# Kernel optimization log

Measured on AMD Instinct MI355X. Metric: run time of the kernel, lower is better.

## Reference

```python
import jax, jax.numpy as jnp
import numpy as np

HIDDEN = 1280
NUM_HEADS = 16
HEAD_DIM = HIDDEN // NUM_HEADS  # 80
ROPE_DIM = HEAD_DIM // 2        # 40
THETA = 10000.0
SEQ = 3072


def setup_inputs() -> dict:
    key = jax.random.key(0)
    ks = jax.random.split(key, 6)
    hidden_states = jax.random.normal(ks[0], (SEQ, HIDDEN), dtype=jnp.float32)
    position_ids = jax.random.randint(ks[1], (SEQ, 2), 0, 64, dtype=jnp.int32)
    qkv_w = jax.random.normal(ks[2], (HIDDEN, 3 * HIDDEN), dtype=jnp.float32) * (HIDDEN ** -0.5)
    qkv_b = jax.random.normal(ks[3], (3 * HIDDEN,), dtype=jnp.float32) * 0.02
    o_w = jax.random.normal(ks[4], (HIDDEN, HIDDEN), dtype=jnp.float32) * (HIDDEN ** -0.5)
    o_b = jax.random.normal(ks[5], (HIDDEN,), dtype=jnp.float32) * 0.02
    return {"hidden_states": hidden_states, "position_ids": position_ids,
            "qkv_w": qkv_w, "qkv_b": qkv_b, "o_w": o_w, "o_b": o_b}


def _rotate_half(x):
    x1, x2 = jnp.split(x, 2, axis=-1)
    return jnp.concatenate([-x2, x1], axis=-1)


def reference(hidden_states, position_ids, qkv_w, qkv_b, o_w, o_b):
    seq_len = hidden_states.shape[0]
    # fused QKV projection
    qkv = hidden_states @ qkv_w + qkv_b                     # (S, 3*H*D)
    qkv = qkv.reshape(seq_len, 3, NUM_HEADS, HEAD_DIM)
    q, k, v = qkv[:, 0], qkv[:, 1], qkv[:, 2]               # each (S, h, d)
    # 2D RoPE: inv_freq over rope dim = head_dim // 2
    inv_freq = 1.0 / (THETA ** (jnp.arange(0, ROPE_DIM, 2, dtype=jnp.float32) / ROPE_DIM))
    pos = position_ids.astype(jnp.float32)
    h_freqs = jnp.outer(pos[:, 0], inv_freq)                # (S, rope/2)
    w_freqs = jnp.outer(pos[:, 1], inv_freq)                # (S, rope/2)
    freqs = jnp.concatenate([h_freqs, w_freqs], axis=-1)    # (S, rope)
    emb = jnp.concatenate([freqs, freqs], axis=-1)          # (S, head_dim)
    cos = jnp.cos(emb)[:, None, :]                          # (S, 1, d)
    sin = jnp.sin(emb)[:, None, :]
    q = q * cos + _rotate_half(q) * sin
    k = k * cos + _rotate_half(k) * sin
    # manual attention
    scaling = HEAD_DIM ** -0.5
    attn = jnp.einsum('qhd,khd->hqk', q * scaling, k)       # (h, S, S)
    attn = jax.nn.softmax(attn, axis=-1)
    out = jnp.einsum('hqk,khd->qhd', attn, v)               # (S, h, d)
    out = out.reshape(seq_len, HIDDEN)
    return out @ o_w + o_b
```

## Files before the change

### kernel.cpp

```cpp
#include <hip/hip_runtime.h>

#define SEQ  3072
#define HID  1280
#define NH   16
#define HD   80
#define NQKV 3840

typedef unsigned short u16;
typedef unsigned int u32;
typedef __attribute__((ext_vector_type(8))) short short8;
typedef __attribute__((ext_vector_type(4))) float floatx4;

__device__ __forceinline__ u16 f2bf(float x) {
    u32 u = __float_as_uint(x);
    u += 0x7fffu + ((u >> 16) & 1u);
    return (u16)(u >> 16);
}
__device__ __forceinline__ float bf2f(u16 b) {
    return __uint_as_float(((u32)b) << 16);
}
__device__ __forceinline__ u32 pack2bf(float a, float b) {
    u32 ua = __float_as_uint(a) + 0x8000u;
    u32 ub = __float_as_uint(b) + 0x8000u;
    return (ua >> 16) | (ub & 0xffff0000u);
}

typedef const __attribute__((address_space(1))) unsigned int* gp1_t;
typedef __attribute__((address_space(3))) unsigned int* lp3_t;
__device__ __forceinline__ void gld16(const void* g, void* l) {
    __builtin_amdgcn_global_load_lds((gp1_t)g, (lp3_t)l, 16, 0, 0);
}

__device__ __forceinline__ int swz_qk(int c, int r) {
    return (c < 8) ? (c ^ (r & 7)) : (8 + ((c - 8) ^ (r & 3)));
}

__global__ void rope_tables_k(const int* __restrict__ pos, float* __restrict__ cosb,
                              float* __restrict__ sinb) {
    int s = blockIdx.x;
    int j = threadIdx.x;
    if (j >= 40) return;
    float p = (float)((j < 20) ? pos[s * 2] : pos[s * 2 + 1]);
    int i = (j < 20) ? j : j - 20;
    float inv = powf(10000.0f, -(float)i / 20.0f);
    float a = p * inv;
    cosb[s * 40 + j] = cosf(a);
    sinb[s * 40 + j] = sinf(a);
}

__global__ void cast_bf16_k(const float* __restrict__ x, u16* __restrict__ hi, int n) {
    int i = blockIdx.x * 256 + threadIdx.x;
    if (i >= n) return;
    hi[i] = f2bf(x[i]);
}

__global__ void transpose_cast_k(const float* __restrict__ w, u16* __restrict__ thi,
                                 int K, int N) {
    __shared__ float tile[32][33];
    int n0 = blockIdx.x * 32, k0 = blockIdx.y * 32;
    int c = threadIdx.x & 31, r8 = threadIdx.x >> 5;
    for (int rr = r8; rr < 32; rr += 8)
        tile[rr][c] = w[(size_t)(k0 + rr) * N + n0 + c];
    __syncthreads();
    for (int rr = r8; rr < 32; rr += 8)
        thi[(size_t)(n0 + rr) * K + k0 + c] = f2bf(tile[c][rr]);
}

__global__ __launch_bounds__(256, 3) void gemm_bf16_k(
    const u16* __restrict__ A, const u16* __restrict__ B,
    const float* __restrict__ bias, float* __restrict__ C,
    int M, int N, int K) {
    __shared__ u16 lA[128 * 64], lB[128 * 64];
    const int t = threadIdx.x, lane = t & 63, w = t >> 6;
    const int qi = lane & 15, quad = lane >> 4;
    const int m0 = blockIdx.y * 128, n0 = blockIdx.x * 128;
    const int wm = (w >> 1) * 64, wn = (w & 1) * 64;

    floatx4 acc[4][4];
    for (int mi = 0; mi < 4; mi++)
        for (int ni = 0; ni < 4; ni++) acc[mi][ni] = (floatx4){0.f, 0.f, 0.f, 0.f};

    const int rg = lane >> 3;
    const int ce = ((lane & 7) ^ rg) * 8;
    size_t gA[4], gB[4];
    for (int g = 0; g < 4; g++) {
        int row = w * 32 + g * 8 + rg;
        gA[g] = (size_t)(m0 + row) * K + ce;
        gB[g] = (size_t)(n0 + row) * K + ce;
    }

    for (int k0 = 0; k0 < K; k0 += 64) {
        for (int g = 0; g < 4; g++) {
            gld16(A + gA[g] + k0, &lA[(w * 32 + g * 8) * 64]);
            gld16(B + gB[g] + k0, &lB[(w * 32 + g * 8) * 64]);
        }
        __syncthreads();
        short8 af[4][2], bf[4][2];
        for (int mi = 0; mi < 4; mi++) {
            int row = wm + mi * 16 + qi;
            for (int kh = 0; kh < 2; kh++)
                af[mi][kh] = *(const short8*)&lA[row * 64 + (((kh * 4 + quad) ^ (row & 7)) << 3)];
        }
        for (int ni = 0; ni < 4; ni++) {
            int row = wn + ni * 16 + qi;
            for (int kh = 0; kh < 2; kh++)
                bf[ni][kh] = *(const short8*)&lB[row * 64 + (((kh * 4 + quad) ^ (row & 7)) << 3)];
        }
        for (int mi = 0; mi < 4; mi++)
            for (int ni = 0; ni < 4; ni++) {
                acc[mi][ni] = __builtin_amdgcn_mfma_f32_16x16x32_bf16(af[mi][0], bf[ni][0], acc[mi][ni], 0, 0, 0);
                acc[mi][ni] = __builtin_amdgcn_mfma_f32_16x16x32_bf16(af[mi][1], bf[ni][1], acc[mi][ni], 0, 0, 0);
            }
        __syncthreads();
    }
    for (int mi = 0; mi < 4; mi++)
        for (int ni = 0; ni < 4; ni++) {
            int col = n0 + wn + ni * 16 + qi;
            int rowb = m0 + wm + mi * 16 + quad * 4;
            float b = bias[col];
            for (int r = 0; r < 4; r++)
                C[(size_t)(rowb + r) * N + col] = acc[mi][ni][r] + b;
        }
}

__global__ void pack_qkv_k(const float* __restrict__ qkv, const float* __restrict__ cosb,
                           const float* __restrict__ sinb,
                           u16* __restrict__ Qs, u16* __restrict__ Ks, u16* __restrict__ Vs) {
    __shared__ float lv[80 * 65];
    const int t = threadIdx.x;
    const int h = blockIdx.y, s0 = blockIdx.x * 64;
    const float scale = 0.11180339887498949f;

    for (int i = t; i < 64 * 40; i += 256) {
        int rl = i / 40, j = i % 40;
        int s = s0 + rl;
        float c = cosb[s * 40 + j], sn = sinb[s * 40 + j];
        const float* qb = qkv + (size_t)s * NQKV + h * HD;
        float q1 = qb[j], q2 = qb[j + 40];
        size_t base = (size_t)(h * SEQ + s) * 96;
        int j2 = j + 40;
        size_t o1 = base + swz_qk(j >> 3, s) * 8 + (j & 7);
        size_t o2 = base + swz_qk(j2 >> 3, s) * 8 + (j2 & 7);
        Qs[o1] = f2bf((q1 * c - q2 * sn) * scale);
        Qs[o2] = f2bf((q2 * c + q1 * sn) * scale);
        const float* kb = qb + HID;
        float k1 = kb[j], k2 = kb[j + 40];
        Ks[o1] = f2bf(k1 * c - k2 * sn);
        Ks[o2] = f2bf(k2 * c + k1 * sn);
    }
    for (int i = t; i < 64 * 16; i += 256) {
        int rl = i / 16, jj = 80 + i % 16;
        int s = s0 + rl;
        size_t o = (size_t)(h * SEQ + s) * 96 + swz_qk(jj >> 3, s) * 8 + (jj & 7);
        Qs[o] = 0;
        Ks[o] = 0;
    }
    for (int i = t; i < 64 * 80; i += 256) {
        int rl = i / 80, d = i % 80;
        lv[d * 65 + rl] = qkv[(size_t)(s0 + rl) * NQKV + 2 * HID + h * HD + d];
    }
    __syncthreads();
    for (int i = t; i < 80 * 64; i += 256) {
        int d = i / 64, c2l = i % 64;
        int pc = ((c2l >> 3) ^ (d & 7));
        Vs[((size_t)h * HD + d) * SEQ + s0 + pc * 8 + (c2l & 7)] = f2bf(lv[d * 65 + c2l]);
    }
}

__global__ __launch_bounds__(256, 3) void attn_k(
    const u16* __restrict__ Qs, const u16* __restrict__ Ks, const u16* __restrict__ Vs,
    float* __restrict__ Op, float* __restrict__ lp) {
    __shared__ u16 kbuf[2][6144];
    __shared__ u16 vbuf[2][5120];
    __shared__ u16 pls[4][1024];

    const int t = threadIdx.x, lane = t & 63, w = t >> 6;
    const int qi = lane & 15, quad = lane >> 4;
    const int h = blockIdx.y, q0 = blockIdx.x * 128, ksp = blockIdx.z;
    const int kc0 = ksp * (SEQ / 2);
    u16* const kflat = &kbuf[0][0];

    {
        const u16* Qt = Qs + (size_t)(h * SEQ + q0) * 96;
        for (int j = 0; j < 6; j++) {
            int o = (w * 6 + j) * 512;
            gld16(Qt + o + lane * 8, kflat + o);
        }
    }
    __syncthreads();
    short8 bq[2][3];
    for (int qg = 0; qg < 2; qg++) {
        int row = w * 32 + qg * 16 + qi;
        for (int k3 = 0; k3 < 3; k3++) {
            int p = (k3 < 2) ? ((4 * k3 + quad) ^ (qi & 7)) : (8 + (quad ^ (qi & 3)));
            bq[qg][k3] = *(const short8*)&kflat[(row * 12 + p) * 8];
        }
    }
    __syncthreads();

    float l_lane[2] = {0.f, 0.f};
    floatx4 acco[2][5];
    for (int qg = 0; qg < 2; qg++)
        for (int dt = 0; dt < 5; dt++) acco[qg][dt] = (floatx4){0.f, 0.f, 0.f, 0.f};

    auto stage = [&](int it, int buf) {
        int kc = kc0 + it * 64;
        const u16* Kt = Ks + (size_t)(h * SEQ + kc) * 96;
        for (int j = 0; j < 3; j++) {
            int o = (w * 3 + j) * 512;
            gld16(Kt + o + lane * 8, &kbuf[buf][o]);
        }
        const u16* Vt = Vs + (size_t)h * HD * SEQ + kc;
        for (int i = w; i < 10; i += 4) {
            int p16 = i * 64 + lane;
            int d = p16 >> 3, pc = p16 & 7;
            gld16(Vt + (size_t)d * SEQ + pc * 8, &vbuf[buf][i * 512]);
        }
    };
    stage(0, 0);
    __syncthreads();

    const int NT = (SEQ / 2) / 64;
    char* const myp = (char*)&pls[w][0];
    for (int it = 0; it < NT; it++) {
        int cur = it & 1;
        if (it + 1 < NT) stage(it + 1, cur ^ 1);
        const u16* kb = &kbuf[cur][0];
        const u16* vb = &vbuf[cur][0];
        for (int c2 = 0; c2 < 2; c2++) {
            for (int ktl = 0; ktl < 2; ktl++) {
                int kt = c2 * 2 + ktl;
                int arow = kt * 16 + qi;
                short8 ak[3];
                for (int k3 = 0; k3 < 3; k3++) {
                    int p = (k3 < 2) ? ((4 * k3 + quad) ^ (qi & 7)) : (8 + (quad ^ (qi & 3)));
                    ak[k3] = *(const short8*)&kb[(arow * 12 + p) * 8];
                }
                for (int qg = 0; qg < 2; qg++) {
                    floatx4 s = (floatx4){0.f, 0.f, 0.f, 0.f};
                    s = __builtin_amdgcn_mfma_f32_16x16x32_bf16(ak[0], bq[qg][0], s, 0, 0, 0);
                    s = __builtin_amdgcn_mfma_f32_16x16x32_bf16(ak[1], bq[qg][1], s, 0, 0, 0);
                    s = __builtin_amdgcn_mfma_f32_16x16x32_bf16(ak[2], bq[qg][2], s, 0, 0, 0);
                    float e0 = __expf(s[0]), e1 = __expf(s[1]);
                    float e2 = __expf(s[2]), e3 = __expf(s[3]);
                    l_lane[qg] += (e0 + e1) + (e2 + e3);
                    uint2 pk;
                    pk.x = pack2bf(e0, e1);
                    pk.y = pack2bf(e2, e3);
                    int u = 2 * ktl + (quad >> 1);
                    *(uint2*)(myp + qg * 1024 + qi * 64 + ((u ^ (qi & 3)) << 4) + ((quad & 1) << 3)) = pk;
                }
            }
            short8 bp0 = *(const short8*)(myp + qi * 64 + ((quad ^ (qi & 3)) << 4));
            short8 bp1 = *(const short8*)(myp + 1024 + qi * 64 + ((quad ^ (qi & 3)) << 4));
            int pv = (4 * c2 + quad) ^ (qi & 7);
            for (int dt = 0; dt < 5; dt++) {
                short8 av = *(const short8*)&vb[((dt * 16 + qi) * 8 + pv) * 8];
                acco[0][dt] = __builtin_amdgcn_mfma_f32_16x16x32_bf16(av, bp0, acco[0][dt], 0, 0, 0);
                acco[1][dt] = __builtin_amdgcn_mfma_f32_16x16x32_bf16(av, bp1, acco[1][dt], 0, 0, 0);
            }
        }
        __syncthreads();
    }

    for (int qg = 0; qg < 2; qg++) {
        float lq = l_lane[qg];
        lq += __shfl_xor(lq, 16);
        lq += __shfl_xor(lq, 32);
        int q = q0 + w * 32 + qg * 16 + qi;
        if (quad == 0) lp[(size_t)(ksp * NH + h) * SEQ + q] = lq;
        for (int dt = 0; dt < 5; dt++)
            for (int r = 0; r < 4; r++) {
                int d = dt * 16 + quad * 4 + r;
                Op[((size_t)(ksp * NH + h) * HD + d) * SEQ + q] = acco[qg][dt][r];
            }
    }
}

__global__ void merge_k(const float* __restrict__ Op, const float* __restrict__ lp,
                        u16* __restrict__ att) {
    __shared__ float ls[HD * 65];
    __shared__ float li[64];
    const int t = threadIdx.x;
    const int h = blockIdx.y, q0 = blockIdx.x * 64;
    for (int i = t; i < HD * 64; i += 256) {
        int d = i / 64, ql = i % 64;
        size_t a0 = ((size_t)h * HD + d) * SEQ + q0 + ql;
        size_t a1 = ((size_t)(NH + h) * HD + d) * SEQ + q0 + ql;
        ls[d * 65 + ql] = Op[a0] + Op[a1];
    }
    if (t < 64)
        li[t] = 1.0f / (lp[(size_t)h * SEQ + q0 + t] + lp[(size_t)(NH + h) * SEQ + q0 + t]);
    __syncthreads();
    for (int i = t; i < 64 * HD; i += 256) {
        int ql = i / HD, d = i % HD;
        att[(size_t)(q0 + ql) * HID + h * HD + d] = f2bf(ls[d * 65 + ql] * li[ql]);
    }
}

extern "C" void kernel_launch(void* const* d_in, const int* in_sizes, int n_in,
                              void* d_out, int out_size, void* d_ws, size_t ws_size,
                              hipStream_t stream) {
    const float* hs   = (const float*)d_in[0];
    const int*   pos  = (const int*)d_in[1];
    const float* qkvw = (const float*)d_in[2];
    const float* qkvb = (const float*)d_in[3];
    const float* ow   = (const float*)d_in[4];
    const float* ob   = (const float*)d_in[5];
    float* out = (float*)d_out;

    char* p = (char*)d_ws;
    auto alloc = [&](size_t bytes) {
        char* r = p;
        p += (bytes + 255) & ~(size_t)255;
        return r;
    };
    float* cosb = (float*)alloc((size_t)SEQ * 40 * 4);
    float* sinb = (float*)alloc((size_t)SEQ * 40 * 4);
    u16* owT = (u16*)alloc((size_t)HID * HID * 2);
    char* pool1 = alloc(18874368 + 9437184);
    u16* hH = (u16*)pool1;
    u16* wT = (u16*)(pool1 + 7864320);
    u16* Qs = (u16*)pool1;
    u16* Ks = (u16*)(pool1 + 9437184);
    char* pool2 = alloc((size_t)SEQ * NQKV * 4);
    float* qkv_s = (float*)pool2;
    u16* att  = (u16*)pool2;
    float* Op = (float*)(pool2 + 7864320);
    float* lp = (float*)(pool2 + 39321600);
    u16* Vs = (u16*)alloc((size_t)NH * HD * SEQ * 2);

    hipLaunchKernelGGL(rope_tables_k, dim3(SEQ), dim3(64), 0, stream, pos, cosb, sinb);
    hipLaunchKernelGGL(cast_bf16_k, dim3((SEQ * HID + 255) / 256), dim3(256), 0, stream,
                       hs, hH, SEQ * HID);
    hipLaunchKernelGGL(transpose_cast_k, dim3(NQKV / 32, HID / 32), dim3(256), 0, stream,
                       qkvw, wT, HID, NQKV);
    hipLaunchKernelGGL(transpose_cast_k, dim3(HID / 32, HID / 32), dim3(256), 0, stream,
                       ow, owT, HID, HID);
    hipLaunchKernelGGL(gemm_bf16_k, dim3(NQKV / 128, SEQ / 128), dim3(256), 0, stream,
                       hH, wT, qkvb, qkv_s, SEQ, NQKV, HID);
    hipLaunchKernelGGL(pack_qkv_k, dim3(SEQ / 64, NH), dim3(256), 0, stream,
                       qkv_s, cosb, sinb, Qs, Ks, Vs);
    hipLaunchKernelGGL(attn_k, dim3(SEQ / 128, NH, 2), dim3(256), 0, stream,
                       Qs, Ks, Vs, Op, lp);
    hipLaunchKernelGGL(merge_k, dim3(SEQ / 64, NH), dim3(256), 0, stream, Op, lp, att);
    hipLaunchKernelGGL(gemm_bf16_k, dim3(HID / 128, SEQ / 128), dim3(256), 0, stream,
                       att, owT, ob, out, SEQ, HID, HID);
}
```

Before: 256.9 us.

## Vectorize pack/merge kernels, use exp2 with folded log2e, rework P LDS swizzle

Vectorizes the QKV packing, V transpose and merge kernels with float4 loads and packed bf16 stores instead of scalar element accesses. Folds log2(e) into the Q scale so the attention kernel can call the hardware exp2 directly. The P-tile round-trip through LDS now uses a perm-based truncating bf16 pack and a wider 128-byte row swizzle, and the Q/K tail-chunk swizzle changes to avoid LDS bank conflicts. The perm pack truncates instead of rounding, a small accuracy change, while the other conversions switch to round-to-nearest-even.

```diff
diff --git a/kernel.cpp b/kernel.cpp
--- a/kernel.cpp
+++ b/kernel.cpp
@@ -16,13 +16,8 @@
     u += 0x7fffu + ((u >> 16) & 1u);
     return (u16)(u >> 16);
 }
-__device__ __forceinline__ float bf2f(u16 b) {
-    return __uint_as_float(((u32)b) << 16);
-}
-__device__ __forceinline__ u32 pack2bf(float a, float b) {
-    u32 ua = __float_as_uint(a) + 0x8000u;
-    u32 ub = __float_as_uint(b) + 0x8000u;
-    return (ua >> 16) | (ub & 0xffff0000u);
+__device__ __forceinline__ u32 packrne(float a, float b) {
+    return (u32)f2bf(a) | ((u32)f2bf(b) << 16);
 }
 
 typedef const __attribute__((address_space(1))) unsigned int* gp1_t;
@@ -32,7 +27,7 @@
 }
 
 __device__ __forceinline__ int swz_qk(int c, int r) {
-    return (c < 8) ? (c ^ (r & 7)) : (8 + ((c - 8) ^ (r & 3)));
+    return (c < 8) ? (c ^ (r & 7)) : (8 + ((c - 8) ^ ((r >> 1) & 3)));
 }
 
 __global__ void rope_tables_k(const int* __restrict__ pos, float* __restrict__ cosb,
@@ -129,41 +124,61 @@
     __shared__ float lv[80 * 65];
     const int t = threadIdx.x;
     const int h = blockIdx.y, s0 = blockIdx.x * 64;
-    const float scale = 0.11180339887498949f;
-
-    for (int i = t; i < 64 * 40; i += 256) {
-        int rl = i / 40, j = i % 40;
+    const float qsc = 0.11180339887498949f * 1.4426950408889634f;
+
+    for (int i = t; i < 64 * 10; i += 256) {
+        int rl = i / 10, jg = i % 10;
+        int s = s0 + rl, j = jg * 4;
+        const float4 cc = *(const float4*)&cosb[s * 40 + j];
+        const float4 ss = *(const float4*)&sinb[s * 40 + j];
+        const float* qb = qkv + (size_t)s * NQKV + h * HD;
+        const float4 q1 = *(const float4*)&qb[j];
+        const float4 q2 = *(const float4*)&qb[j + 40];
+        const float* kb = qb + HID;
+        const float4 k1 = *(const float4*)&kb[j];
+        const float4 k2 = *(const float4*)&kb[j + 40];
+        uint2 qo1, qo2, ko1, ko2;
+        qo1.x = packrne((q1.x * cc.x - q2.x * ss.x) * qsc, (q1.y * cc.y - q2.y * ss.y) * qsc);
+        qo1.y = packrne((q1.z * cc.z - q2.z * ss.z) * qsc, (q1.w * cc.w - q2.w * ss.w) * qsc);
+        qo2.x = packrne((q2.x * cc.x + q1.x * ss.x) * qsc, (q2.y * cc.y + q1.y * ss.y) * qsc);
+        qo2.y = packrne((q2.z * cc.z + q1.z * ss.z) * qsc, (q2.w * cc.w + q1.w * ss.w) * qsc);
+        ko1.x = packrne(k1.x * cc.x - k2.x * ss.x, k1.y * cc.y - k2.y * ss.y);
+        ko1.y = packrne(k1.z * cc.z - k2.z * ss.z, k1.w * cc.w - k2.w * ss.w);
+        ko2.x = packrne(k2.x * cc.x + k1.x * ss.x, k2.y * cc.y + k1.y * ss.y);
+        ko2.y = packrne(k2.z * cc.z + k1.z * ss.z, k2.w * cc.w + k1.w * ss.w);
+        size_t base = (size_t)(h * SEQ + s) * 96;
+        int c0 = j >> 3, sub0 = j & 7;
+        int c1 = (j + 40) >> 3, sub1 = (j + 40) & 7;
+        int p0 = swz_qk(c0, s);
+        int p1 = swz_qk(c1, s);
+        *(uint2*)&Qs[base + p0 * 8 + sub0] = qo1;
+        *(uint2*)&Qs[base + p1 * 8 + sub1] = qo2;
+        *(uint2*)&Ks[base + p0 * 8 + sub0] = ko1;
+        *(uint2*)&Ks[base + p1 * 8 + sub1] = ko2;
+    }
+    for (int i = t; i < 64 * 2; i += 256) {
+        int rl = i >> 1, cz = 10 + (i & 1);
         int s = s0 + rl;
-        float c = cosb[s * 40 + j], sn = sinb[s * 40 + j];
-        const float* qb = qkv + (size_t)s * NQKV + h * HD;
-        float q1 = qb[j], q2 = qb[j + 40];
+        int pz = swz_qk(cz, s);
         size_t base = (size_t)(h * SEQ + s) * 96;
-        int j2 = j + 40;
-        size_t o1 = base + swz_qk(j >> 3, s) * 8 + (j & 7);
-        size_t o2 = base + swz_qk(j2 >> 3, s) * 8 + (j2 & 7);
-        Qs[o1] = f2bf((q1 * c - q2 * sn) * scale);
-        Qs[o2] = f2bf((q2 * c + q1 * sn) * scale);
-        const float* kb = qb + HID;
-        float k1 = kb[j], k2 = kb[j + 40];
-        Ks[o1] = f2bf(k1 * c - k2 * sn);
-        Ks[o2] = f2bf(k2 * c + k1 * sn);
-    }
-    for (int i = t; i < 64 * 16; i += 256) {
-        int rl = i / 16, jj = 80 + i % 16;
-        int s = s0 + rl;
-        size_t o = (size_t)(h * SEQ + s) * 96 + swz_qk(jj >> 3, s) * 8 + (jj & 7);
-        Qs[o] = 0;
-        Ks[o] = 0;
+        *(uint4*)&Qs[base + pz * 8] = (uint4){0, 0, 0, 0};
+        *(uint4*)&Ks[base + pz * 8] = (uint4){0, 0, 0, 0};
     }
     for (int i = t; i < 64 * 80; i += 256) {
         int rl = i / 80, d = i % 80;
         lv[d * 65 + rl] = qkv[(size_t)(s0 + rl) * NQKV + 2 * HID + h * HD + d];
     }
     __syncthreads();
-    for (int i = t; i < 80 * 64; i += 256) {
-        int d = i / 64, c2l = i % 64;
-        int pc = ((c2l >> 3) ^ (d & 7));
-        Vs[((size_t)h * HD + d) * SEQ + s0 + pc * 8 + (c2l & 7)] = f2bf(lv[d * 65 + c2l]);
+    for (int i = t; i < 80 * 16; i += 256) {
+        int d = i / 16, g = i % 16;
+        int c2l = g * 4;
+        float v0 = lv[d * 65 + c2l], v1 = lv[d * 65 + c2l + 1];
+        float v2 = lv[d * 65 + c2l + 2], v3 = lv[d * 65 + c2l + 3];
+        int pc = (g >> 1) ^ (d & 7);
+        uint2 o;
+        o.x = packrne(v0, v1);
+        o.y = packrne(v2, v3);
+        *(uint2*)&Vs[((size_t)h * HD + d) * SEQ + s0 + pc * 8 + (g & 1) * 4] = o;
     }
 }
 
@@ -192,7 +207,7 @@
     for (int qg = 0; qg < 2; qg++) {
         int row = w * 32 + qg * 16 + qi;
         for (int k3 = 0; k3 < 3; k3++) {
-            int p = (k3 < 2) ? ((4 * k3 + quad) ^ (qi & 7)) : (8 + (quad ^ (qi & 3)));
+            int p = (k3 < 2) ? ((4 * k3 + quad) ^ (qi & 7)) : (8 + (quad ^ ((qi >> 1) & 3)));
             bq[qg][k3] = *(const short8*)&kflat[(row * 12 + p) * 8];
         }
     }
@@ -233,7 +248,7 @@
                 int arow = kt * 16 + qi;
                 short8 ak[3];
                 for (int k3 = 0; k3 < 3; k3++) {
-                    int p = (k3 < 2) ? ((4 * k3 + quad) ^ (qi & 7)) : (8 + (quad ^ (qi & 3)));
+                    int p = (k3 < 2) ? ((4 * k3 + quad) ^ (qi & 7)) : (8 + (quad ^ ((qi >> 1) & 3)));
                     ak[k3] = *(const short8*)&kb[(arow * 12 + p) * 8];
                 }
                 for (int qg = 0; qg < 2; qg++) {
@@ -241,18 +256,20 @@
                     s = __builtin_amdgcn_mfma_f32_16x16x32_bf16(ak[0], bq[qg][0], s, 0, 0, 0);
                     s = __builtin_amdgcn_mfma_f32_16x16x32_bf16(ak[1], bq[qg][1], s, 0, 0, 0);
                     s = __builtin_amdgcn_mfma_f32_16x16x32_bf16(ak[2], bq[qg][2], s, 0, 0, 0);
-                    float e0 = __expf(s[0]), e1 = __expf(s[1]);
-                    float e2 = __expf(s[2]), e3 = __expf(s[3]);
+                    float e0 = __builtin_amdgcn_exp2f(s[0]);
+                    float e1 = __builtin_amdgcn_exp2f(s[1]);
+                    float e2 = __builtin_amdgcn_exp2f(s[2]);
+                    float e3 = __builtin_amdgcn_exp2f(s[3]);
                     l_lane[qg] += (e0 + e1) + (e2 + e3);
                     uint2 pk;
-                    pk.x = pack2bf(e0, e1);
-                    pk.y = pack2bf(e2, e3);
-                    int u = 2 * ktl + (quad >> 1);
-                    *(uint2*)(myp + qg * 1024 + qi * 64 + ((u ^ (qi & 3)) << 4) + ((quad & 1) << 3)) = pk;
+                    pk.x = __builtin_amdgcn_perm(__float_as_uint(e1), __float_as_uint(e0), 0x07060302u);
+                    pk.y = __builtin_amdgcn_perm(__float_as_uint(e3), __float_as_uint(e2), 0x07060302u);
+                    int chunk = qg * 4 + 2 * ktl + (quad >> 1);
+                    *(uint2*)(myp + qi * 128 + ((chunk ^ (qi & 7)) << 4) + ((quad & 1) << 3)) = pk;
                 }
             }
-            short8 bp0 = *(const short8*)(myp + qi * 64 + ((quad ^ (qi & 3)) << 4));
-            short8 bp1 = *(const short8*)(myp + 1024 + qi * 64 + ((quad ^ (qi & 3)) << 4));
+            short8 bp0 = *(const short8*)(myp + qi * 128 + (((quad) ^ (qi & 7)) << 4));
+            short8 bp1 = *(const short8*)(myp + qi * 128 + (((4 + quad) ^ (qi & 7)) << 4));
             int pv = (4 * c2 + quad) ^ (qi & 7);
             for (int dt = 0; dt < 5; dt++) {
                 short8 av = *(const short8*)&vb[((dt * 16 + qi) * 8 + pv) * 8];
@@ -283,18 +300,26 @@
     __shared__ float li[64];
     const int t = threadIdx.x;
     const int h = blockIdx.y, q0 = blockIdx.x * 64;
-    for (int i = t; i < HD * 64; i += 256) {
-        int d = i / 64, ql = i % 64;
-        size_t a0 = ((size_t)h * HD + d) * SEQ + q0 + ql;
-        size_t a1 = ((size_t)(NH + h) * HD + d) * SEQ + q0 + ql;
-        ls[d * 65 + ql] = Op[a0] + Op[a1];
+    for (int i = t; i < HD * 16; i += 256) {
+        int d = i / 16, g = i % 16;
+        size_t a0 = ((size_t)h * HD + d) * SEQ + q0 + g * 4;
+        size_t a1 = ((size_t)(NH + h) * HD + d) * SEQ + q0 + g * 4;
+        const float4 v0 = *(const float4*)&Op[a0];
+        const float4 v1 = *(const float4*)&Op[a1];
+        ls[d * 65 + g * 4 + 0] = v0.x + v1.x;
+        ls[d * 65 + g * 4 + 1] = v0.y + v1.y;
+        ls[d * 65 + g * 4 + 2] = v0.z + v1.z;
+        ls[d * 65 + g * 4 + 3] = v0.w + v1.w;
     }
     if (t < 64)
         li[t] = 1.0f / (lp[(size_t)h * SEQ + q0 + t] + lp[(size_t)(NH + h) * SEQ + q0 + t]);
     __syncthreads();
-    for (int i = t; i < 64 * HD; i += 256) {
-        int ql = i / HD, d = i % HD;
-        att[(size_t)(q0 + ql) * HID + h * HD + d] = f2bf(ls[d * 65 + ql] * li[ql]);
+    for (int i = t; i < 64 * 40; i += 256) {
+        int ql = i / 40, dg = i % 40;
+        int d0 = dg * 2;
+        float s = li[ql];
+        u32 o = packrne(ls[d0 * 65 + ql] * s, ls[(d0 + 1) * 65 + ql] * s);
+        *(u32*)&att[(size_t)(q0 + ql) * HID + h * HD + d0] = o;
     }
 }
 
```

After: 248.8 us. 1.03x faster.
